# Optimization experiments

Hardware: AMD Instinct MI355X
Metric: run time of the kernel (lower is better)

## Reference

```python
import jax, jax.numpy as jnp
import numpy as np

DIM = 256
HEADS = 8
P = 8   # patch_size
S = 4   # stride


def _pos_index(p):
    # Swin-style relative position index, computed statically in numpy
    coord = np.arange(p)
    ii, jj = np.meshgrid(coord, coord, indexing='ij')
    cf = np.stack([ii.ravel(), jj.ravel()])              # [2, p*p]
    rel = cf[:, :, None] - cf[:, None, :]                # [2, P, P]
    rel = rel.transpose(1, 2, 0).copy()                  # [P, P, 2]
    rel[:, :, 0] += p - 1
    rel[:, :, 1] += p - 1
    rel[:, :, 0] *= 2 * p - 1
    return jnp.asarray(rel.sum(-1))                      # [P, P] int


def setup_inputs() -> dict:
    key = jax.random.key(0)
    k1, k2, k3, k4, k5 = jax.random.split(key, 5)
    x = jax.random.normal(k1, (2, DIM, 96, 96), jnp.float32)
    # depthwise 1x1 conv on 3*dim channels -> per-channel scale + bias
    qkv_w = jax.random.normal(k2, (3 * DIM,), jnp.float32) * 0.1 + 1.0
    qkv_b = jax.random.normal(k3, (3 * DIM,), jnp.float32) * 0.1
    # 1x1 conv dim->dim, no bias
    out_w = jax.random.normal(k4, (DIM, DIM), jnp.float32) * 0.05
    # relative position bias table, trunc_normal(std=0.02)
    pos_table = jax.random.normal(k5, ((2 * P - 1) ** 2, HEADS), jnp.float32) * 0.02
    return {"x": x, "qkv_w": qkv_w, "qkv_b": qkv_b, "out_w": out_w, "pos_table": pos_table}


def reference(x, qkv_w, qkv_b, out_w, pos_table):
    B, C, H, W = x.shape
    h, p, s = HEADS, P, S
    d = C // h
    pad = p - s
    # replicate pad right/bottom
    xp = jnp.pad(x, ((0, 0), (0, 0), (0, pad), (0, pad)), mode='edge')
    x3 = jnp.concatenate([xp, xp, xp], axis=1)           # [B, 3C, Hp, Wp]
    # depthwise 1x1 conv == per-channel affine
    qkv = x3 * qkv_w[None, :, None, None] + qkv_b[None, :, None, None]
    n = (H + pad - p) // s + 1                           # patches per side
    idx = (jnp.arange(n) * s)[:, None] + jnp.arange(p)[None, :]   # [n, p]
    # unfold: extract overlapping p x p patches with stride s
    t = qkv[:, :, idx, :]                                # [B, 3C, n, p, Wp]
    t = t[:, :, :, :, idx]                               # [B, 3C, n, p, n, p]
    t = t.transpose(0, 1, 2, 4, 3, 5)                    # [B, 3C, n, n, p, p]
    t = t.reshape(B, 3, h, d, n * n, p * p).transpose(1, 0, 2, 4, 5, 3)  # [3,B,h,N,P,d]
    q, k, v = t[0] * (d ** -0.5), t[1], t[2]
    bias = pos_table[_pos_index(p)]                      # [P, P, h]
    bias = bias.transpose(2, 0, 1)                       # [h, P, P]
    attn = jnp.einsum('bhnqd,bhnkd->bhnqk', q, k) + bias[None, :, None]
    attn = jax.nn.softmax(attn, axis=-1)
    out = jnp.einsum('bhnqk,bhnkd->bhnqd', attn, v)      # [B, h, N, P, d]
    # keep only the top-left stride x stride of each patch, then fold (non-overlap)
    out = out.reshape(B, h, n, n, p, p, d)[:, :, :, :, :s, :s]   # [B,h,n,n,s,s,d]
    out = out.transpose(0, 1, 6, 2, 4, 3, 5).reshape(B, C, H, W)
    return jnp.einsum('oc,bchw->bohw', out_w, out)
```

## Files before the change

### kernel.cpp

```cpp
#include <hip/hip_runtime.h>

typedef float f4 __attribute__((ext_vector_type(4)));
typedef float f32x4 __attribute__((ext_vector_type(4)));
typedef __bf16 bf16x8 __attribute__((ext_vector_type(8)));
typedef __bf16 bf16x4 __attribute__((ext_vector_type(4)));

#define NPSIDE 24

#define XS(ch_, r_, c_) xs[(ch_) * 253 + (r_) * 21 + (c_)]

__global__ __launch_bounds__(512, 2) void patch_attn(
    const float* __restrict__ x,
    const float* __restrict__ qkv_w,
    const float* __restrict__ qkv_b,
    const float* __restrict__ pos_table,
    const float* __restrict__ wmat,
    __bf16* __restrict__ mid,
    __bf16* __restrict__ wbf)
{
    __shared__ float xs[32 * 253];
    __shared__ __bf16 Ps[8][16][72];

    const int t = threadIdx.x;

    if (blockIdx.x < 32) {
        const int i = (blockIdx.x * 512 + t) * 4;
        const int o = i >> 8, c = i & 255;
        const f4 v = *(const f4*)&wmat[i];
        bf16x4 ov;
        #pragma unroll
        for (int j = 0; j < 4; ++j) ov[j] = (__bf16)v[j];
        *(bf16x4*)&wbf[((o >> 4) * 8 + (c >> 5)) * 512 + (o & 15) * 32 + (c & 31)] = ov;
    }

    int raw = blockIdx.x;
    const int sw = (raw & 7) * 144 + (raw >> 3);
    const int pgrp = sw % 72;
    const int bh   = sw / 72;
    const int head = bh & 7;
    const int b    = bh >> 3;
    const int ni0  = (pgrp / 6) * 2;
    const int nj0  = (pgrp % 6) * 4;
    const int c0   = head * 32;

    if (t < 384) {
        const int ch  = t / 12;
        const int row = t % 12;
        const int rg  = min(4 * ni0 + row, 95);
        const float* xrow = x + (((size_t)b * 256 + c0 + ch) * 96 + rg) * 96;
        float* xdst = &XS(ch, row, 0);
        const int cb = 4 * nj0;
        #pragma unroll
        for (int cg = 0; cg < 5; ++cg) {
            const int cg4 = cb + cg * 4;
            f4 v;
            if (cg4 <= 92) {
                v = *(const f4*)&xrow[cg4];
            } else {
                f4 u = *(const f4*)&xrow[92];
                v = (f4){u.w, u.w, u.w, u.w};
            }
            xdst[cg * 4 + 0] = v.x;
            xdst[cg * 4 + 1] = v.y;
            xdst[cg * 4 + 2] = v.z;
            xdst[cg * 4 + 3] = v.w;
        }
    }

    const int wv = t >> 6, l = t & 63;
    const int l16 = l & 15, lg = l >> 4;
    const float qscale = 0.17677669529663687f;

    float kw8[8], kb8[8], qw8[8], qb8[8];
    #pragma unroll
    for (int j = 0; j < 8; ++j) {
        const int c = c0 + 8 * lg + j;
        kw8[j] = qkv_w[256 + c];
        kb8[j] = qkv_b[256 + c];
        qw8[j] = qkv_w[c] * qscale;
        qb8[j] = qkv_b[c] * qscale;
    }
    float vw2[2], vb2[2];
    #pragma unroll
    for (int nt = 0; nt < 2; ++nt) {
        const int c = c0 + nt * 16 + l16;
        vw2[nt] = qkv_w[512 + c];
        vb2[nt] = qkv_b[512 + c];
    }

    __syncthreads();

    const int wni = wv >> 2, wnj = wv & 3;
    const int ni = ni0 + wni, nj = nj0 + wnj;
    const int rb = 4 * wni, cbl = 4 * wnj;

    bf16x8 qf;
    {
        const int qrow = rb + (l16 >> 2), qcol = cbl + (l16 & 3);
        #pragma unroll
        for (int j = 0; j < 8; ++j)
            qf[j] = (__bf16)(XS(8 * lg + j, qrow, qcol) * qw8[j] + qb8[j]);
    }

    const f32x4 zf = {0.f, 0.f, 0.f, 0.f};
    f32x4 sacc[4];
    #pragma unroll
    for (int t4 = 0; t4 < 4; ++t4) {
        const int px = l16 + 16 * t4;
        const int kr = rb + (px >> 3), kc = cbl + (px & 7);
        bf16x8 kf;
        #pragma unroll
        for (int j = 0; j < 8; ++j)
            kf[j] = (__bf16)(XS(8 * lg + j, kr, kc) * kw8[j] + kb8[j]);
        sacc[t4] = __builtin_amdgcn_mfma_f32_16x16x32_bf16(qf, kf, zf, 0, 0, 0);
    }

    float sv[4][4], rinv[4];
    #pragma unroll
    for (int r = 0; r < 4; ++r) {
        const int qrow = lg * 4 + r;
        const int qi = qrow >> 2, qj = qrow & 3;
        float m = -1e30f;
        #pragma unroll
        for (int t4 = 0; t4 < 4; ++t4) {
            const int kcol = l16 + 16 * t4;
            const int ki = kcol >> 3, kj = kcol & 7;
            const float s = sacc[t4][r]
                + pos_table[((qi - ki + 7) * 15 + (qj - kj + 7)) * 8 + head];
            sv[t4][r] = s;
            m = fmaxf(m, s);
        }
        #pragma unroll
        for (int off = 8; off >= 1; off >>= 1)
            m = fmaxf(m, __shfl_xor(m, off, 16));
        float sum = 0.f;
        #pragma unroll
        for (int t4 = 0; t4 < 4; ++t4) {
            const float p = __expf(sv[t4][r] - m);
            sv[t4][r] = p;
            sum += p;
        }
        #pragma unroll
        for (int off = 8; off >= 1; off >>= 1)
            sum += __shfl_xor(sum, off, 16);
        rinv[r] = 1.0f / sum;
        #pragma unroll
        for (int t4 = 0; t4 < 4; ++t4)
            Ps[wv][qrow][l16 + 16 * t4] = (__bf16)sv[t4][r];
    }

    f32x4 oa = zf, ob = zf;
    #pragma unroll
    for (int kt = 0; kt < 2; ++kt) {
        bf16x8 pf = *(const bf16x8*)&Ps[wv][l16][lg * 8 + 32 * kt];
        bf16x8 v0, v1;
        #pragma unroll
        for (int j = 0; j < 8; ++j) {
            const int px = kt * 32 + 8 * lg + j;
            const int vr = rb + (px >> 3), vc = cbl + (px & 7);
            v0[j] = (__bf16)(XS(l16,      vr, vc) * vw2[0] + vb2[0]);
            v1[j] = (__bf16)(XS(16 + l16, vr, vc) * vw2[1] + vb2[1]);
        }
        oa = __builtin_amdgcn_mfma_f32_16x16x32_bf16(pf, v0, oa, 0, 0, 0);
        ob = __builtin_amdgcn_mfma_f32_16x16x32_bf16(pf, v1, ob, 0, 0, 0);
    }

    const int pbase = ni * 384 + lg * 96 + nj * 4;
    __bf16* mbb = mid + (size_t)b * 9216 * 256;
    #pragma unroll
    for (int r = 0; r < 4; ++r) {
        const int p = pbase + r;
        __bf16* dst = mbb + ((p >> 4) * 8 + head) * 512 + (p & 15) * 32;
        dst[l16]      = (__bf16)(oa[r] * rinv[r]);
        dst[16 + l16] = (__bf16)(ob[r] * rinv[r]);
    }
}

__global__ __launch_bounds__(256) void proj(
    const __bf16* __restrict__ wbf,
    const __bf16* __restrict__ mid,
    float* __restrict__ y)
{
    __shared__ __align__(16) __bf16 wlds[2][8][512];

    const int t  = threadIdx.x;
    const int wv = t >> 6;
    const int l  = t & 63;
    const int l16 = l & 15, lg = l >> 4;
    const int fragoff = l16 * 32 + lg * 8;

    int raw = blockIdx.x;
    const int sw  = (raw & 7) * 144 + (raw >> 3);
    const int ptg = sw >> 3;
    const int og2 = sw & 7;
    const int pt  = ptg * 4 + wv;
    const int ot0 = og2 * 2;
    const int b   = blockIdx.z;

    {
        const bf16x8* wsrc = (const bf16x8*)&wbf[(size_t)ot0 * 8 * 512];
        bf16x8* wdst = (bf16x8*)&wlds[0][0][0];
        #pragma unroll
        for (int i = 0; i < 4; ++i)
            wdst[t + 256 * i] = wsrc[t + 256 * i];
    }
    __syncthreads();

    const __bf16* midb = mid + (size_t)b * 9216 * 256;

    f32x4 acc0 = {0.f, 0.f, 0.f, 0.f}, acc1 = {0.f, 0.f, 0.f, 0.f};

    #pragma unroll
    for (int kt = 0; kt < 8; ++kt) {
        const bf16x8 bfr =
            *(const bf16x8*)&midb[(size_t)(pt * 8 + kt) * 512 + fragoff];
        const bf16x8 af0 = *(const bf16x8*)&wlds[0][kt][fragoff];
        const bf16x8 af1 = *(const bf16x8*)&wlds[1][kt][fragoff];
        acc0 = __builtin_amdgcn_mfma_f32_16x16x32_bf16(af0, bfr, acc0, 0, 0, 0);
        acc1 = __builtin_amdgcn_mfma_f32_16x16x32_bf16(af1, bfr, acc1, 0, 0, 0);
    }

    const int p = pt * 16 + l16;
    #pragma unroll
    for (int ot = 0; ot < 2; ++ot) {
        const f32x4 a = ot ? acc1 : acc0;
        const int o = (ot0 + ot) * 16 + lg * 4;
        float* yb = y + ((size_t)b * 256 + o) * 9216 + p;
        #pragma unroll
        for (int r = 0; r < 4; ++r)
            yb[(size_t)r * 9216] = a[r];
    }
}

extern "C" void kernel_launch(void* const* d_in, const int* in_sizes, int n_in,
                              void* d_out, int out_size, void* d_ws, size_t ws_size,
                              hipStream_t stream) {
    const float* x         = (const float*)d_in[0];
    const float* qkv_w     = (const float*)d_in[1];
    const float* qkv_b     = (const float*)d_in[2];
    const float* out_w     = (const float*)d_in[3];
    const float* pos_table = (const float*)d_in[4];
    float* y    = (float*)d_out;
    __bf16* mid = (__bf16*)d_ws;
    __bf16* wbf = (__bf16*)((char*)d_ws + (12u << 20));

    patch_attn<<<dim3(1152), dim3(512), 0, stream>>>(
        x, qkv_w, qkv_b, pos_table, out_w, mid, wbf);
    proj<<<dim3(1152, 1, 2), dim3(256), 0, stream>>>(
        wbf, mid, y);
}
```

Before: 37.03 us.

## Precompute Q/K/V affine in bf16 LDS layouts for vector fragment loads

Rather than staging raw fp32 x in shared memory and applying the per-channel affine for each MFMA fragment element, threads now apply the Q, K and V affine once during the global load. They store bf16 results into dedicated LDS arrays laid out so each MFMA fragment is a single 16-byte load. This removes repeated scalar LDS reads, FMAs and conversions that came from overlapping patches reusing the same pixels, and it halves LDS footprint per element. Risks include padded layouts with possible bank conflicts, and global loads now 8-byte per channel row instead of 16-byte vectors.

```diff
diff --git a/kernel.cpp b/kernel.cpp
--- a/kernel.cpp
+++ b/kernel.cpp
@@ -1,13 +1,13 @@
 #include <hip/hip_runtime.h>
 
 typedef float f4 __attribute__((ext_vector_type(4)));
+typedef float f2 __attribute__((ext_vector_type(2)));
 typedef float f32x4 __attribute__((ext_vector_type(4)));
 typedef __bf16 bf16x8 __attribute__((ext_vector_type(8)));
 typedef __bf16 bf16x4 __attribute__((ext_vector_type(4)));
+typedef __bf16 bf16x2 __attribute__((ext_vector_type(2)));
 
 #define NPSIDE 24
-
-#define XS(ch_, r_, c_) xs[(ch_) * 253 + (r_) * 21 + (c_)]
 
 __global__ __launch_bounds__(512, 2) void patch_attn(
     const float* __restrict__ x,
@@ -18,7 +18,9 @@
     __bf16* __restrict__ mid,
     __bf16* __restrict__ wbf)
 {
-    __shared__ float xs[32 * 253];
+    __shared__ __bf16 Kreg[240][40];
+    __shared__ __bf16 Qreg[128][40];
+    __shared__ __bf16 Vreg[32][292];
     __shared__ __bf16 Ps[8][16][72];
 
     const int t = threadIdx.x;
@@ -42,76 +44,66 @@
     const int ni0  = (pgrp / 6) * 2;
     const int nj0  = (pgrp % 6) * 4;
     const int c0   = head * 32;
-
-    if (t < 384) {
-        const int ch  = t / 12;
-        const int row = t % 12;
+    const float qscale = 0.17677669529663687f;
+
+    if (t < 480) {
+        const int pxp = t % 120;
+        const int chg = t / 120;
+        const int px0 = 2 * pxp;
+        const int row = px0 / 20, col = px0 % 20;
         const int rg  = min(4 * ni0 + row, 95);
-        const float* xrow = x + (((size_t)b * 256 + c0 + ch) * 96 + rg) * 96;
-        float* xdst = &XS(ch, row, 0);
-        const int cb = 4 * nj0;
-        #pragma unroll
-        for (int cg = 0; cg < 5; ++cg) {
-            const int cg4 = cb + cg * 4;
-            f4 v;
-            if (cg4 <= 92) {
-                v = *(const f4*)&xrow[cg4];
+        const int cg  = 4 * nj0 + col;
+        const bool own = (row < 8) && (col < 16);
+        const float* xb = x + ((size_t)(b * 256 + c0 + 8 * chg) * 96 + rg) * 96;
+
+        bf16x8 kv0, kv1, qv0, qv1;
+        #pragma unroll
+        for (int j = 0; j < 8; ++j) {
+            const int c = c0 + 8 * chg + j;
+            const float kw = qkv_w[256 + c], kb = qkv_b[256 + c];
+            const float vw = qkv_w[512 + c], vb = qkv_b[512 + c];
+            const float qw = qkv_w[c] * qscale, qb = qkv_b[c] * qscale;
+            f2 xv;
+            if (cg <= 94) {
+                xv = *(const f2*)&xb[(size_t)j * 9216 + cg];
             } else {
-                f4 u = *(const f4*)&xrow[92];
-                v = (f4){u.w, u.w, u.w, u.w};
+                const float s = xb[(size_t)j * 9216 + 95];
+                xv.x = s; xv.y = s;
             }
-            xdst[cg * 4 + 0] = v.x;
-            xdst[cg * 4 + 1] = v.y;
-            xdst[cg * 4 + 2] = v.z;
-            xdst[cg * 4 + 3] = v.w;
-        }
-    }
+            kv0[j] = (__bf16)(xv.x * kw + kb);
+            kv1[j] = (__bf16)(xv.y * kw + kb);
+            bf16x2 vv;
+            vv[0] = (__bf16)(xv.x * vw + vb);
+            vv[1] = (__bf16)(xv.y * vw + vb);
+            *(bf16x2*)&Vreg[8 * chg + j][row * 24 + col] = vv;
+            qv0[j] = (__bf16)(xv.x * qw + qb);
+            qv1[j] = (__bf16)(xv.y * qw + qb);
+        }
+        *(bf16x8*)&Kreg[px0][8 * chg]     = kv0;
+        *(bf16x8*)&Kreg[px0 + 1][8 * chg] = kv1;
+        if (own) {
+            const int qpx = row * 16 + col;
+            *(bf16x8*)&Qreg[qpx][8 * chg]     = qv0;
+            *(bf16x8*)&Qreg[qpx + 1][8 * chg] = qv1;
+        }
+    }
+    __syncthreads();
 
     const int wv = t >> 6, l = t & 63;
     const int l16 = l & 15, lg = l >> 4;
-    const float qscale = 0.17677669529663687f;
-
-    float kw8[8], kb8[8], qw8[8], qb8[8];
-    #pragma unroll
-    for (int j = 0; j < 8; ++j) {
-        const int c = c0 + 8 * lg + j;
-        kw8[j] = qkv_w[256 + c];
-        kb8[j] = qkv_b[256 + c];
-        qw8[j] = qkv_w[c] * qscale;
-        qb8[j] = qkv_b[c] * qscale;
-    }
-    float vw2[2], vb2[2];
-    #pragma unroll
-    for (int nt = 0; nt < 2; ++nt) {
-        const int c = c0 + nt * 16 + l16;
-        vw2[nt] = qkv_w[512 + c];
-        vb2[nt] = qkv_b[512 + c];
-    }
-
-    __syncthreads();
-
     const int wni = wv >> 2, wnj = wv & 3;
     const int ni = ni0 + wni, nj = nj0 + wnj;
     const int rb = 4 * wni, cbl = 4 * wnj;
 
-    bf16x8 qf;
-    {
-        const int qrow = rb + (l16 >> 2), qcol = cbl + (l16 & 3);
-        #pragma unroll
-        for (int j = 0; j < 8; ++j)
-            qf[j] = (__bf16)(XS(8 * lg + j, qrow, qcol) * qw8[j] + qb8[j]);
-    }
-
     const f32x4 zf = {0.f, 0.f, 0.f, 0.f};
+    const bf16x8 qf =
+        *(const bf16x8*)&Qreg[(rb + (l16 >> 2)) * 16 + cbl + (l16 & 3)][lg * 8];
     f32x4 sacc[4];
     #pragma unroll
     for (int t4 = 0; t4 < 4; ++t4) {
-        const int px = l16 + 16 * t4;
-        const int kr = rb + (px >> 3), kc = cbl + (px & 7);
-        bf16x8 kf;
-        #pragma unroll
-        for (int j = 0; j < 8; ++j)
-            kf[j] = (__bf16)(XS(8 * lg + j, kr, kc) * kw8[j] + kb8[j]);
+        const int ppx = l16 + 16 * t4;
+        const int rpx = (rb + (ppx >> 3)) * 20 + cbl + (ppx & 7);
+        const bf16x8 kf = *(const bf16x8*)&Kreg[rpx][lg * 8];
         sacc[t4] = __builtin_amdgcn_mfma_f32_16x16x32_bf16(qf, kf, zf, 0, 0, 0);
     }
 
@@ -152,15 +144,10 @@
     f32x4 oa = zf, ob = zf;
     #pragma unroll
     for (int kt = 0; kt < 2; ++kt) {
-        bf16x8 pf = *(const bf16x8*)&Ps[wv][l16][lg * 8 + 32 * kt];
-        bf16x8 v0, v1;
-        #pragma unroll
-        for (int j = 0; j < 8; ++j) {
-            const int px = kt * 32 + 8 * lg + j;
-            const int vr = rb + (px >> 3), vc = cbl + (px & 7);
-            v0[j] = (__bf16)(XS(l16,      vr, vc) * vw2[0] + vb2[0]);
-            v1[j] = (__bf16)(XS(16 + l16, vr, vc) * vw2[1] + vb2[1]);
-        }
+        const bf16x8 pf = *(const bf16x8*)&Ps[wv][l16][lg * 8 + 32 * kt];
+        const int voff = (rb + 4 * kt + lg) * 24 + cbl;
+        const bf16x8 v0 = *(const bf16x8*)&Vreg[l16][voff];
+        const bf16x8 v1 = *(const bf16x8*)&Vreg[16 + l16][voff];
         oa = __builtin_amdgcn_mfma_f32_16x16x32_bf16(pf, v0, oa, 0, 0, 0);
         ob = __builtin_amdgcn_mfma_f32_16x16x32_bf16(pf, v1, ob, 0, 0, 0);
     }
```

New measurement: 38.81 us. 1.05x slower.
